# Optimization experiments

Measured on AMD Instinct MI355X. Metric: run time of the kernel, lower is better.

## Reference

```python
import jax, jax.numpy as jnp
import numpy as np
import math

NUM_HEADS = 12
LAMBDA_INIT = 0.8 - 0.6 * math.exp(-0.3 * (2 - 1))  # lambda_init(depth=2)
SIGMA = 0.5


def _feature_map(t):
    # f(x) = x + 1 if x >= 0 else exp(x)  (ELU+1 style)
    return jnp.where(t >= 0, t + 1.0, jnp.exp(t))


def setup_inputs() -> dict:
    key = jax.random.key(0)
    ks = jax.random.split(key, 9)
    B_, N, C, H = 2048, 64, 384, NUM_HEADS
    d = C // H
    s = 0.02
    return {
        "x": jax.random.normal(ks[0], (B_, N, C), dtype=jnp.float32),
        "qkv_w": jax.random.normal(ks[1], (C, 3 * C), dtype=jnp.float32) * s,
        "qkv_b": jax.random.normal(ks[2], (3 * C,), dtype=jnp.float32) * s,
        "proj_w": jax.random.normal(ks[3], (C, C), dtype=jnp.float32) * s,
        "proj_b": jax.random.normal(ks[4], (C,), dtype=jnp.float32) * s,
        "lambda_k1": jax.random.normal(ks[5], (H, d), dtype=jnp.float32) * 0.1,
        "lambda_v1": jax.random.normal(ks[6], (H, d), dtype=jnp.float32) * 0.1,
        "lambda_k2": jax.random.normal(ks[7], (H, d), dtype=jnp.float32) * 0.1,
        "lambda_v2": jax.random.normal(ks[8], (H, d), dtype=jnp.float32) * 0.1,
    }


def reference(x, qkv_w, qkv_b, proj_w, proj_b,
              lambda_k1, lambda_v1, lambda_k2, lambda_v2):
    B_, N, C = x.shape
    H = NUM_HEADS
    d = C // H
    scale = d ** -0.5

    # qkv projection -> (3, B_, H, N, d)
    qkv = (x @ qkv_w + qkv_b).reshape(B_, N, 3, H, d).transpose(2, 0, 3, 1, 4)
    q, k, v = qkv[0], qkv[1], qkv[2]
    q = q * scale

    # dual-lambda gating: per-head scalar
    lam1 = jnp.exp(jnp.sum(lambda_k1 * lambda_v1, axis=-1))  # (H,)
    lam2 = jnp.exp(jnp.sum(lambda_k2 * lambda_v2, axis=-1))  # (H,)
    lambda_full = lam1 - lam2 + LAMBDA_INIT                   # (H,)

    # feature maps on K^T (B_,H,d,N) and V (B_,H,N,d)
    fk = _feature_map(jnp.swapaxes(k, -1, -2))  # (B_, H, d, N)
    fv = _feature_map(v)                         # (B_, H, N, d)

    # gaussian decay over feature-index pairs (d, d)
    idx = jnp.arange(d, dtype=jnp.float32)
    gauss = jnp.exp(-((idx[:, None] - idx[None, :]) ** 2) / (2.0 * SIGMA ** 2))

    # K^T V products with gaussian decay; key1==key2, value1==value2 in source
    A = jnp.einsum('bhdn,bhne->bhde', fk, fv) * gauss  # (B_, H, d, d)
    attn = A - lambda_full[None, :, None, None] * A

    out = jnp.einsum('bhnd,bhde->bhne', q, attn)       # (B_, H, N, d)
    out = jnp.swapaxes(out, 1, 2).reshape(B_, N, C)
    return out @ proj_w + proj_b
```

## Files before the change

kernel.cpp:

```cpp
#include <hip/hip_runtime.h>
#include <hip/hip_bf16.h>
#include <math.h>


typedef __attribute__((ext_vector_type(8))) short short8;
typedef __attribute__((ext_vector_type(4))) float f32x4;
typedef __attribute__((ext_vector_type(4))) unsigned short us4;

typedef const __attribute__((address_space(1))) unsigned int gu32c;
typedef __attribute__((address_space(3))) unsigned int lu32;

#define MFMA_BF16(A,B,C) __builtin_amdgcn_mfma_f32_16x16x32_bf16(A,B,C,0,0,0)

__device__ __forceinline__ unsigned short f2bf(float f) {
  unsigned int u = __float_as_uint(f);
  u += 0x7FFFu + ((u >> 16) & 1u);
  return (unsigned short)(u >> 16);
}

#define BB 2048
#define NN 64
#define CC 384
#define HH 12
#define DD 32

#define WS_WT   0
#define WS_W2T  884736
#define WS_WB   1179648
#define WS_LAM  1184256

__global__ void setup_kernel(const float* __restrict__ qkv_w,
                             const float* __restrict__ qkv_b,
                             const float* __restrict__ proj_w,
                             const float* __restrict__ lk1, const float* __restrict__ lv1,
                             const float* __restrict__ lk2, const float* __restrict__ lv2,
                             unsigned short* __restrict__ WT,
                             unsigned short* __restrict__ W2T,
                             float* __restrict__ Wb,
                             float* __restrict__ lamS)
{
  const int nWT  = HH * 96 * CC;
  const int nW2T = CC * CC;
  const int nWb  = HH * 96;
  int gid = blockIdx.x * 256 + threadIdx.x;
  if (gid < nWT) {
    int h = gid / (96 * CC);
    int r = gid % (96 * CC);
    int c = r / CC;
    int k = r % CC;
    int col = (c >> 5) * CC + h * DD + (c & 31);
    WT[gid] = f2bf(qkv_w[(size_t)k * (3 * CC) + col]);
  } else if (gid < nWT + nW2T) {
    int j = gid - nWT;
    int n = j / CC, k = j % CC;
    W2T[j] = f2bf(proj_w[(size_t)k * CC + n]);
  } else if (gid < nWT + nW2T + nWb) {
    int j = gid - nWT - nW2T;
    int h = j / 96, c = j % 96;
    Wb[j] = qkv_b[(c >> 5) * CC + h * DD + (c & 31)];
  } else if (gid < nWT + nW2T + nWb + HH) {
    int h = gid - nWT - nW2T - nWb;
    float s1 = 0.f, s2 = 0.f;
    for (int i = 0; i < DD; ++i) {
      s1 += lk1[h * DD + i] * lv1[h * DD + i];
      s2 += lk2[h * DD + i] * lv2[h * DD + i];
    }
    float lambda_init = 0.8f - 0.6f * __expf(-0.3f);
    float lam = __expf(s1) - __expf(s2) + lambda_init;
    lamS[h] = 1.0f - lam;
  }
}

__global__ __launch_bounds__(512, 2) void fused_kernel(
    const float* __restrict__ x,
    const unsigned short* __restrict__ WT,
    const float* __restrict__ Wb,
    const float* __restrict__ lamS,
    const unsigned short* __restrict__ W2T,
    const float* __restrict__ proj_b,
    float* __restrict__ out)
{
  __shared__ __align__(16) char smem[144384];
  unsigned short* OX       = (unsigned short*)smem;
  unsigned short* WtRegion = (unsigned short*)(smem + 100352);
  unsigned short* Sq       = (unsigned short*)(smem + 124928);
  unsigned short* AtBase   = (unsigned short*)(smem + 139264);

  const int tid  = threadIdx.x;
  const int lane = tid & 63;
  const int wave = tid >> 6;
  const int quad = lane >> 4;
  const int l15  = lane & 15;
  const int rg   = wave >> 1;
  const int ch   = wave & 1;
  const int bb   = wave >> 2;
  const int ww   = wave & 3;

  auto stage_wt = [&](const unsigned short* src0, char* ldsb) {
    {
      int c = tid >> 3, sg = tid & 7;
      const unsigned short* sp = src0 + c * CC + ((sg ^ (c & 7)) << 3);
      __builtin_amdgcn_global_load_lds((gu32c*)(const void*)sp,
          (lu32*)(void*)(ldsb + (tid & ~63) * 16), 16, 0, 0);
    }
    if (tid < 256) {
      int p = 512 + tid;
      int c = p >> 3, sg = p & 7;
      const unsigned short* sp = src0 + c * CC + ((sg ^ (c & 7)) << 3);
      __builtin_amdgcn_global_load_lds((gu32c*)(const void*)sp,
          (lu32*)(void*)(ldsb + 8192 + (tid & ~63) * 16), 16, 0, 0);
    }
  };

  auto stage_w2 = [&](int nh, int kc, int sel) {
    char* ldsb = (char*)WtRegion + sel * 12288;
    {
      int row = tid >> 2, sg = tid & 3;
      const unsigned short* sp = W2T + (size_t)(nh * 192 + row) * CC + kc * 32
                                 + ((sg ^ ((row >> 1) & 3)) << 3);
      __builtin_amdgcn_global_load_lds((gu32c*)(const void*)sp,
          (lu32*)(void*)(ldsb + (tid & ~63) * 16), 16, 0, 0);
    }
    if (tid < 256) {
      int p = 512 + tid;
      int row = p >> 2, sg = p & 3;
      const unsigned short* sp = W2T + (size_t)(nh * 192 + row) * CC + kc * 32
                                 + ((sg ^ ((row >> 1) & 3)) << 3);
      __builtin_amdgcn_global_load_lds((gu32c*)(const void*)sp,
          (lu32*)(void*)(ldsb + (p & ~63) * 16), 16, 0, 0);
    }
  };

  stage_wt(WT, (char*)WtRegion);
  {
    const float* xb = x + (size_t)blockIdx.x * (2 * NN * CC);
    #pragma unroll
    for (int it = 0; it < 24; ++it) {
      int i = it * 512 + tid;
      int row = i / 96, c4 = i % 96;
      float4 v = *(const float4*)(xb + row * CC + c4 * 4);
      ushort4 o;
      o.x = f2bf(v.x); o.y = f2bf(v.y); o.z = f2bf(v.z); o.w = f2bf(v.w);
      *(ushort4*)(OX + row * 392 + c4 * 4) = o;
    }
  }
  __syncthreads();

  short8 xa[2][12];
  #pragma unroll
  for (int mt = 0; mt < 2; ++mt)
    #pragma unroll
    for (int s = 0; s < 12; ++s)
      xa[mt][s] = *(const short8*)(OX + (rg * 32 + mt * 16 + l15) * 392
                                   + s * 32 + quad * 8);

  for (int h = 0; h < HH; ++h) {
    const unsigned short* Wh = WT + (size_t)h * (96 * CC);

    f32x4 acc[2][3];
    #pragma unroll
    for (int mt = 0; mt < 2; ++mt)
      #pragma unroll
      for (int t = 0; t < 3; ++t) acc[mt][t] = (f32x4){0.f, 0.f, 0.f, 0.f};

    #pragma unroll
    for (int kc = 0; kc < 6; ++kc) {
      if (kc < 5)
        stage_wt(Wh + (kc + 1) * 64, (char*)WtRegion + ((kc + 1) & 1) * 12288);
      const unsigned short* Wt = WtRegion + (kc & 1) * 6144;
      __builtin_amdgcn_s_setprio(1);
      #pragma unroll
      for (int step = 0; step < 2; ++step) {
        const int sw = (((step * 4 + quad) ^ (l15 & 7)) << 3);
        #pragma unroll
        for (int t = 0; t < 3; ++t) {
          short8 bfr = *(const short8*)(Wt + (ch * 48 + t * 16 + l15) * 64 + sw);
          acc[0][t] = MFMA_BF16(xa[0][kc * 2 + step], bfr, acc[0][t]);
          acc[1][t] = MFMA_BF16(xa[1][kc * 2 + step], bfr, acc[1][t]);
        }
      }
      __builtin_amdgcn_s_setprio(0);
      __syncthreads();
    }

    {
      unsigned short* StK = WtRegion + bb * 4608;
      unsigned short* StV = StK + 2304;
      #pragma unroll
      for (int mt = 0; mt < 2; ++mt) {
        const int rowb = rg * 32 + mt * 16 + quad * 4;
        const int nloc = rowb & 63;
        #pragma unroll
        for (int t = 0; t < 3; ++t) {
          const int c0 = ch * 48 + t * 16;
          const int c  = c0 + l15;
          float bias = Wb[h * 96 + c];
          if (c0 < 32) {
            #pragma unroll
            for (int r = 0; r < 4; ++r) {
              float v = (acc[mt][t][r] + bias) * 0.17677669529663689f;
              Sq[(rowb + r) * 56 + c] = f2bf(v);
            }
          } else {
            us4 pk;
            #pragma unroll
            for (int r = 0; r < 4; ++r) {
              float v = acc[mt][t][r] + bias;
              v = (v >= 0.f) ? (v + 1.f) : __expf(v);
              pk[r] = f2bf(v);
            }
            if (c0 < 64) *(us4*)(StK + (c0 - 32 + l15) * 72 + nloc) = pk;
            else         *(us4*)(StV + (c0 - 64 + l15) * 72 + nloc) = pk;
          }
        }
      }
    }
    __syncthreads();

    {
      const unsigned short* StK = WtRegion + bb * 4608;
      const unsigned short* StV = StK + 2304;
      const int i0 = (ww & 1) * 16;
      const int e0 = (ww >> 1) * 16;
      f32x4 accA = (f32x4){0.f, 0.f, 0.f, 0.f};
      #pragma unroll
      for (int n0 = 0; n0 < 64; n0 += 32) {
        short8 afr = *(const short8*)(StK + (i0 + l15) * 72 + n0 + quad * 8);
        short8 bfr = *(const short8*)(StV + (e0 + l15) * 72 + n0 + quad * 8);
        accA = MFMA_BF16(afr, bfr, accA);
      }
      const float lsc = lamS[h];
      unsigned short* At = AtBase + bb * 1280;
      const int e = e0 + l15;
      us4 pk;
      #pragma unroll
      for (int r = 0; r < 4; ++r) {
        int i = i0 + quad * 4 + r;
        float diff = (float)(i - e);
        pk[r] = f2bf(accA[r] * lsc * __expf(-2.0f * diff * diff));
      }
      *(us4*)(At + e * 40 + i0 + quad * 4) = pk;
    }
    __syncthreads();

    if (h < HH - 1) stage_wt(WT + (size_t)(h + 1) * (96 * CC), (char*)WtRegion);
    else            stage_w2(0, 0, 0);

    {
      const unsigned short* At = AtBase + bb * 1280;
      short8 aq = *(const short8*)(Sq + (wave * 16 + l15) * 56 + quad * 8);
      const int lrow = wave * 16 + quad * 4;
      #pragma unroll
      for (int t2 = 0; t2 < 2; ++t2) {
        short8 bA = *(const short8*)(At + (t2 * 16 + l15) * 40 + quad * 8);
        f32x4 accO = MFMA_BF16(aq, bA, ((f32x4){0.f, 0.f, 0.f, 0.f}));
        #pragma unroll
        for (int r = 0; r < 4; ++r)
          OX[(lrow + r) * 392 + h * DD + t2 * 16 + l15] = f2bf(accO[r]);
      }
    }
    __syncthreads();
  }

  {
    const int rg2 = wave >> 1;
    const int cg2 = wave & 1;
    const size_t rowg0 = (size_t)blockIdx.x * 128 + rg2 * 32;

    for (int nh = 0; nh < 2; ++nh) {
      f32x4 acc2[2][6];
      #pragma unroll
      for (int mt = 0; mt < 2; ++mt)
        #pragma unroll
        for (int t = 0; t < 6; ++t) acc2[mt][t] = (f32x4){0.f, 0.f, 0.f, 0.f};

      for (int kc = 0; kc < 12; ++kc) {
        if (kc < 11)      stage_w2(nh, kc + 1, (kc + 1) & 1);
        else if (nh == 0) stage_w2(1, 0, 0);
        const unsigned short* Wp = WtRegion + (kc & 1) * 6144;
        __builtin_amdgcn_s_setprio(1);
        short8 a0 = *(const short8*)(OX + (rg2 * 32 +      l15) * 392
                                     + kc * 32 + quad * 8);
        short8 a1 = *(const short8*)(OX + (rg2 * 32 + 16 + l15) * 392
                                     + kc * 32 + quad * 8);
        #pragma unroll
        for (int t = 0; t < 6; ++t) {
          const int row = cg2 * 96 + t * 16 + l15;
          short8 b = *(const short8*)(Wp + row * 32
                                      + ((quad ^ ((row >> 1) & 3)) << 3));
          acc2[0][t] = MFMA_BF16(a0, b, acc2[0][t]);
          acc2[1][t] = MFMA_BF16(a1, b, acc2[1][t]);
        }
        __builtin_amdgcn_s_setprio(0);
        __syncthreads();
      }

      #pragma unroll
      for (int t = 0; t < 6; ++t) {
        const int col = nh * 192 + cg2 * 96 + t * 16 + l15;
        const float bias = proj_b[col];
        #pragma unroll
        for (int mt = 0; mt < 2; ++mt) {
          const size_t row0 = rowg0 + mt * 16 + quad * 4;
          #pragma unroll
          for (int r = 0; r < 4; ++r)
            out[(row0 + r) * CC + col] = acc2[mt][t][r] + bias;
        }
      }
    }
  }
}

extern "C" void kernel_launch(void* const* d_in, const int* in_sizes, int n_in,
                              void* d_out, int out_size, void* d_ws, size_t ws_size,
                              hipStream_t stream) {
  const float* x      = (const float*)d_in[0];
  const float* qkv_w  = (const float*)d_in[1];
  const float* qkv_b  = (const float*)d_in[2];
  const float* proj_w = (const float*)d_in[3];
  const float* proj_b = (const float*)d_in[4];
  const float* lk1    = (const float*)d_in[5];
  const float* lv1    = (const float*)d_in[6];
  const float* lk2    = (const float*)d_in[7];
  const float* lv2    = (const float*)d_in[8];

  char* ws = (char*)d_ws;
  unsigned short* WT  = (unsigned short*)(ws + WS_WT);
  unsigned short* W2T = (unsigned short*)(ws + WS_W2T);
  float* Wb           = (float*)(ws + WS_WB);
  float* lamS         = (float*)(ws + WS_LAM);

  setup_kernel<<<2309, 256, 0, stream>>>(qkv_w, qkv_b, proj_w,
                                         lk1, lv1, lk2, lv2,
                                         WT, W2T, Wb, lamS);
  fused_kernel<<<1024, 512, 0, stream>>>(x, WT, Wb, lamS, W2T, proj_b,
                                         (float*)d_out);
}
```

Baseline: 590.7 us.

## Fuse per-head output projection into head loop with one-batch 256-thread blocks

```diff
diff --git a/kernel.cpp b/kernel.cpp
--- a/kernel.cpp
+++ b/kernel.cpp
@@ -28,6 +28,15 @@
 #define WS_W2T  884736
 #define WS_WB   1179648
 #define WS_LAM  1184256
+
+#define LDS_WT  0
+#define LDS_W2  24576
+#define LDS_SK  49152
+#define LDS_SV  53760
+#define LDS_SQ  58368
+#define LDS_AT  65536
+#define LDS_OH  68096
+#define LDS_TOT 73216
 
 __global__ void setup_kernel(const float* __restrict__ qkv_w,
                              const float* __restrict__ qkv_b,
@@ -71,7 +80,7 @@
   }
 }
 
-__global__ __launch_bounds__(512, 2) void fused_kernel(
+__global__ __launch_bounds__(256, 2) void fused_kernel(
     const float* __restrict__ x,
     const unsigned short* __restrict__ WT,
     const float* __restrict__ Wb,
@@ -80,11 +89,13 @@
     const float* __restrict__ proj_b,
     float* __restrict__ out)
 {
-  __shared__ __align__(16) char smem[144384];
-  unsigned short* OX       = (unsigned short*)smem;
-  unsigned short* WtRegion = (unsigned short*)(smem + 100352);
-  unsigned short* Sq       = (unsigned short*)(smem + 124928);
-  unsigned short* AtBase   = (unsigned short*)(smem + 139264);
+  __shared__ __align__(16) char smem[LDS_TOT];
+  unsigned short* StK = (unsigned short*)(smem + LDS_SK);
+  unsigned short* StV = (unsigned short*)(smem + LDS_SV);
+  unsigned short* Sq  = (unsigned short*)(smem + LDS_SQ);
+  unsigned short* At  = (unsigned short*)(smem + LDS_AT);
+  unsigned short* Oh  = (unsigned short*)(smem + LDS_OH);
+  unsigned short* W2s = (unsigned short*)(smem + LDS_W2);
 
   const int tid  = threadIdx.x;
   const int lane = tid & 63;
@@ -93,66 +104,57 @@
   const int l15  = lane & 15;
   const int rg   = wave >> 1;
   const int ch   = wave & 1;
-  const int bb   = wave >> 2;
-  const int ww   = wave & 3;
 
   auto stage_wt = [&](const unsigned short* src0, char* ldsb) {
-    {
-      int c = tid >> 3, sg = tid & 7;
-      const unsigned short* sp = src0 + c * CC + ((sg ^ (c & 7)) << 3);
-      __builtin_amdgcn_global_load_lds((gu32c*)(const void*)sp,
-          (lu32*)(void*)(ldsb + (tid & ~63) * 16), 16, 0, 0);
-    }
-    if (tid < 256) {
-      int p = 512 + tid;
+    #pragma unroll
+    for (int i = 0; i < 3; ++i) {
+      int p = i * 256 + tid;
       int c = p >> 3, sg = p & 7;
       const unsigned short* sp = src0 + c * CC + ((sg ^ (c & 7)) << 3);
       __builtin_amdgcn_global_load_lds((gu32c*)(const void*)sp,
-          (lu32*)(void*)(ldsb + 8192 + (tid & ~63) * 16), 16, 0, 0);
+          (lu32*)(void*)(ldsb + (p & ~63) * 16), 16, 0, 0);
     }
   };
-
-  auto stage_w2 = [&](int nh, int kc, int sel) {
-    char* ldsb = (char*)WtRegion + sel * 12288;
-    {
-      int row = tid >> 2, sg = tid & 3;
-      const unsigned short* sp = W2T + (size_t)(nh * 192 + row) * CC + kc * 32
-                                 + ((sg ^ ((row >> 1) & 3)) << 3);
+  auto stage_w2 = [&](int h, int part) {
+    #pragma unroll
+    for (int i = 0; i < 2; ++i) {
+      int p = part * 512 + i * 256 + tid;
+      int n = p >> 2, sg = p & 3;
+      const unsigned short* sp = W2T + (size_t)n * CC + h * DD
+                                 + ((sg ^ ((n >> 1) & 3)) << 3);
       __builtin_amdgcn_global_load_lds((gu32c*)(const void*)sp,
-          (lu32*)(void*)(ldsb + (tid & ~63) * 16), 16, 0, 0);
-    }
-    if (tid < 256) {
-      int p = 512 + tid;
-      int row = p >> 2, sg = p & 3;
-      const unsigned short* sp = W2T + (size_t)(nh * 192 + row) * CC + kc * 32
-                                 + ((sg ^ ((row >> 1) & 3)) << 3);
-      __builtin_amdgcn_global_load_lds((gu32c*)(const void*)sp,
-          (lu32*)(void*)(ldsb + (p & ~63) * 16), 16, 0, 0);
+          (lu32*)(void*)(smem + LDS_W2 + (p & ~63) * 16), 16, 0, 0);
     }
   };
 
-  stage_wt(WT, (char*)WtRegion);
+  stage_wt(WT, smem + LDS_WT);
+
+  short8 xa[2][12];
   {
-    const float* xb = x + (size_t)blockIdx.x * (2 * NN * CC);
-    #pragma unroll
-    for (int it = 0; it < 24; ++it) {
-      int i = it * 512 + tid;
-      int row = i / 96, c4 = i % 96;
-      float4 v = *(const float4*)(xb + row * CC + c4 * 4);
-      ushort4 o;
-      o.x = f2bf(v.x); o.y = f2bf(v.y); o.z = f2bf(v.z); o.w = f2bf(v.w);
-      *(ushort4*)(OX + row * 392 + c4 * 4) = o;
-    }
+    const float* xb = x + (size_t)blockIdx.x * (NN * CC);
+    #pragma unroll
+    for (int mt = 0; mt < 2; ++mt)
+      #pragma unroll
+      for (int s = 0; s < 12; ++s) {
+        const float* p = xb + (rg * 32 + mt * 16 + l15) * CC + s * 32 + quad * 8;
+        float4 u0 = *(const float4*)p;
+        float4 u1 = *(const float4*)(p + 4);
+        short8 f;
+        f[0] = (short)f2bf(u0.x); f[1] = (short)f2bf(u0.y);
+        f[2] = (short)f2bf(u0.z); f[3] = (short)f2bf(u0.w);
+        f[4] = (short)f2bf(u1.x); f[5] = (short)f2bf(u1.y);
+        f[6] = (short)f2bf(u1.z); f[7] = (short)f2bf(u1.w);
+        xa[mt][s] = f;
+      }
   }
-  __syncthreads();
-
-  short8 xa[2][12];
+
+  f32x4 acc_out[2][12];
   #pragma unroll
   for (int mt = 0; mt < 2; ++mt)
     #pragma unroll
-    for (int s = 0; s < 12; ++s)
-      xa[mt][s] = *(const short8*)(OX + (rg * 32 + mt * 16 + l15) * 392
-                                   + s * 32 + quad * 8);
+    for (int t = 0; t < 12; ++t) acc_out[mt][t] = (f32x4){0.f, 0.f, 0.f, 0.f};
+
+  __syncthreads();
 
   for (int h = 0; h < HH; ++h) {
     const unsigned short* Wh = WT + (size_t)h * (96 * CC);
@@ -166,15 +168,20 @@
     #pragma unroll
     for (int kc = 0; kc < 6; ++kc) {
       if (kc < 5)
-        stage_wt(Wh + (kc + 1) * 64, (char*)WtRegion + ((kc + 1) & 1) * 12288);
-      const unsigned short* Wt = WtRegion + (kc & 1) * 6144;
+        stage_wt(Wh + (kc + 1) * 64, smem + LDS_WT + ((kc + 1) & 1) * 12288);
+      else if (h < HH - 1)
+        stage_wt(Wh + 96 * CC, smem + LDS_WT);
+      if (kc < 3) stage_w2(h, kc);
+      const unsigned short* Wt = (const unsigned short*)(smem + LDS_WT)
+                                 + (kc & 1) * 6144;
       __builtin_amdgcn_s_setprio(1);
       #pragma unroll
       for (int step = 0; step < 2; ++step) {
-        const int sw = (((step * 4 + quad) ^ (l15 & 7)) << 3);
         #pragma unroll
         for (int t = 0; t < 3; ++t) {
-          short8 bfr = *(const short8*)(Wt + (ch * 48 + t * 16 + l15) * 64 + sw);
+          const int row = ch * 48 + t * 16 + l15;
+          short8 bfr = *(const short8*)(Wt + row * 64
+                                        + (((step * 4 + quad) ^ (l15 & 7)) << 3));
           acc[0][t] = MFMA_BF16(xa[0][kc * 2 + step], bfr, acc[0][t]);
           acc[1][t] = MFMA_BF16(xa[1][kc * 2 + step], bfr, acc[1][t]);
         }
@@ -183,45 +190,38 @@
       __syncthreads();
     }
 
+    #pragma unroll
+    for (int mt = 0; mt < 2; ++mt) {
+      const int rowb = rg * 32 + mt * 16 + quad * 4;
+      #pragma unroll
+      for (int t = 0; t < 3; ++t) {
+        const int c0 = ch * 48 + t * 16;
+        const int c  = c0 + l15;
+        float bias = Wb[h * 96 + c];
+        if (c0 < 32) {
+          #pragma unroll
+          for (int r = 0; r < 4; ++r) {
+            float v = (acc[mt][t][r] + bias) * 0.17677669529663689f;
+            Sq[(rowb + r) * 56 + c] = f2bf(v);
+          }
+        } else {
+          us4 pk;
+          #pragma unroll
+          for (int r = 0; r < 4; ++r) {
+            float v = acc[mt][t][r] + bias;
+            v = (v >= 0.f) ? (v + 1.f) : __expf(v);
+            pk[r] = f2bf(v);
+          }
+          if (c0 < 64) *(us4*)(StK + (c0 - 32 + l15) * 72 + rowb) = pk;
+          else         *(us4*)(StV + (c0 - 64 + l15) * 72 + rowb) = pk;
+        }
+      }
+    }
+    __syncthreads();
+
     {
-      unsigned short* StK = WtRegion + bb * 4608;
-      unsigned short* StV = StK + 2304;
-      #pragma unroll
-      for (int mt = 0; mt < 2; ++mt) {
-        const int rowb = rg * 32 + mt * 16 + quad * 4;
-        const int nloc = rowb & 63;
-        #pragma unroll
-        for (int t = 0; t < 3; ++t) {
-          const int c0 = ch * 48 + t * 16;
-          const int c  = c0 + l15;
-          float bias = Wb[h * 96 + c];
-          if (c0 < 32) {
-            #pragma unroll
-            for (int r = 0; r < 4; ++r) {
-              float v = (acc[mt][t][r] + bias) * 0.17677669529663689f;
-              Sq[(rowb + r) * 56 + c] = f2bf(v);
-            }
-          } else {
-            us4 pk;
-            #pragma unroll
-            for (int r = 0; r < 4; ++r) {
-              float v = acc[mt][t][r] + bias;
-              v = (v >= 0.f) ? (v + 1.f) : __expf(v);
-              pk[r] = f2bf(v);
-            }
-            if (c0 < 64) *(us4*)(StK + (c0 - 32 + l15) * 72 + nloc) = pk;
-            else         *(us4*)(StV + (c0 - 64 + l15) * 72 + nloc) = pk;
-          }
-        }
-      }
-    }
-    __syncthreads();
-
-    {
-      const unsigned short* StK = WtRegion + bb * 4608;
-      const unsigned short* StV = StK + 2304;
-      const int i0 = (ww & 1) * 16;
-      const int e0 = (ww >> 1) * 16;
+      const int i0 = (wave & 1) * 16;
+      const int e0 = (wave >> 1) * 16;
       f32x4 accA = (f32x4){0.f, 0.f, 0.f, 0.f};
       #pragma unroll
       for (int n0 = 0; n0 < 64; n0 += 32) {
@@ -230,7 +230,6 @@
         accA = MFMA_BF16(afr, bfr, accA);
       }
       const float lsc = lamS[h];
-      unsigned short* At = AtBase + bb * 1280;
       const int e = e0 + l15;
       us4 pk;
       #pragma unroll
@@ -243,70 +242,47 @@
     }
     __syncthreads();
 
-    if (h < HH - 1) stage_wt(WT + (size_t)(h + 1) * (96 * CC), (char*)WtRegion);
-    else            stage_w2(0, 0, 0);
-
     {
-      const unsigned short* At = AtBase + bb * 1280;
       short8 aq = *(const short8*)(Sq + (wave * 16 + l15) * 56 + quad * 8);
-      const int lrow = wave * 16 + quad * 4;
       #pragma unroll
       for (int t2 = 0; t2 < 2; ++t2) {
         short8 bA = *(const short8*)(At + (t2 * 16 + l15) * 40 + quad * 8);
-        f32x4 accO = MFMA_BF16(aq, bA, ((f32x4){0.f, 0.f, 0.f, 0.f}));
+        f32x4 accO = MFMA_BF16(bA, aq, ((f32x4){0.f, 0.f, 0.f, 0.f}));
+        us4 pk;
         #pragma unroll
-        for (int r = 0; r < 4; ++r)
-          OX[(lrow + r) * 392 + h * DD + t2 * 16 + l15] = f2bf(accO[r]);
-      }
+        for (int r = 0; r < 4; ++r) pk[r] = f2bf(accO[r]);
+        *(us4*)(Oh + (wave * 16 + l15) * 40 + t2 * 16 + quad * 4) = pk;
+      }
+    }
+    __syncthreads();
+
+    {
+      __builtin_amdgcn_s_setprio(1);
+      short8 a0 = *(const short8*)(Oh + (rg * 32 +      l15) * 40 + quad * 8);
+      short8 a1 = *(const short8*)(Oh + (rg * 32 + 16 + l15) * 40 + quad * 8);
+      #pragma unroll
+      for (int t = 0; t < 12; ++t) {
+        const int n = ch * 192 + t * 16 + l15;
+        short8 b = *(const short8*)(W2s + n * 32
+                                    + ((quad ^ ((n >> 1) & 3)) << 3));
+        acc_out[0][t] = MFMA_BF16(a0, b, acc_out[0][t]);
+        acc_out[1][t] = MFMA_BF16(a1, b, acc_out[1][t]);
+      }
+      __builtin_amdgcn_s_setprio(0);
     }
     __syncthreads();
   }
 
-  {
-    const int rg2 = wave >> 1;
-    const int cg2 = wave & 1;
-    const size_t rowg0 = (size_t)blockIdx.x * 128 + rg2 * 32;
-
-    for (int nh = 0; nh < 2; ++nh) {
-      f32x4 acc2[2][6];
-      #pragma unroll
-      for (int mt = 0; mt < 2; ++mt)
-        #pragma unroll
-        for (int t = 0; t < 6; ++t) acc2[mt][t] = (f32x4){0.f, 0.f, 0.f, 0.f};
-
-      for (int kc = 0; kc < 12; ++kc) {
-        if (kc < 11)      stage_w2(nh, kc + 1, (kc + 1) & 1);
-        else if (nh == 0) stage_w2(1, 0, 0);
-        const unsigned short* Wp = WtRegion + (kc & 1) * 6144;
-        __builtin_amdgcn_s_setprio(1);
-        short8 a0 = *(const short8*)(OX + (rg2 * 32 +      l15) * 392
-                                     + kc * 32 + quad * 8);
-        short8 a1 = *(const short8*)(OX + (rg2 * 32 + 16 + l15) * 392
-                                     + kc * 32 + quad * 8);
-        #pragma unroll
-        for (int t = 0; t < 6; ++t) {
-          const int row = cg2 * 96 + t * 16 + l15;
-          short8 b = *(const short8*)(Wp + row * 32
-                                      + ((quad ^ ((row >> 1) & 3)) << 3));
-          acc2[0][t] = MFMA_BF16(a0, b, acc2[0][t]);
-          acc2[1][t] = MFMA_BF16(a1, b, acc2[1][t]);
-        }
-        __builtin_amdgcn_s_setprio(0);
-        __syncthreads();
-      }
-
-      #pragma unroll
-      for (int t = 0; t < 6; ++t) {
-        const int col = nh * 192 + cg2 * 96 + t * 16 + l15;
-        const float bias = proj_b[col];
-        #pragma unroll
-        for (int mt = 0; mt < 2; ++mt) {
-          const size_t row0 = rowg0 + mt * 16 + quad * 4;
-          #pragma unroll
-          for (int r = 0; r < 4; ++r)
-            out[(row0 + r) * CC + col] = acc2[mt][t][r] + bias;
-        }
-      }
+  #pragma unroll
+  for (int t = 0; t < 12; ++t) {
+    const int col = ch * 192 + t * 16 + l15;
+    const float bias = proj_b[col];
+    #pragma unroll
+    for (int mt = 0; mt < 2; ++mt) {
+      const size_t row0 = (size_t)blockIdx.x * NN + rg * 32 + mt * 16 + quad * 4;
+      #pragma unroll
+      for (int r = 0; r < 4; ++r)
+        out[(row0 + r) * CC + col] = acc_out[mt][t][r] + bias;
     }
   }
 }
@@ -333,6 +309,6 @@
   setup_kernel<<<2309, 256, 0, stream>>>(qkv_w, qkv_b, proj_w,
                                          lk1, lv1, lk2, lv2,
                                          WT, W2T, Wb, lamS);
-  fused_kernel<<<1024, 512, 0, stream>>>(x, WT, Wb, lamS, W2T, proj_b,
+  fused_kernel<<<2048, 256, 0, stream>>>(x, WT, Wb, lamS, W2T, proj_b,
                                          (float*)d_out);
 }
```

New measurement: 717.4 us. +21.4%, slower.
